# Performance work log

Hardware: AMD Instinct MI355X
Metric: run time of the kernel (lower is better)

The kernel has to match this reference:

```python
import jax, jax.numpy as jnp
import numpy as np

B, C, H, W = 32, 64, 128, 128

def setup_inputs() -> dict:
    key = jax.random.key(0)
    k1, k2, k3, k4 = jax.random.split(key, 4)
    x = jax.random.normal(k1, (B, C, H, W), dtype=jnp.float32)
    theta = jax.random.normal(k2, (C, C), dtype=jnp.float32) * (6.0 / (C + C)) ** 0.5  # xavier-ish
    W_lin = jax.random.normal(k3, (C, C), dtype=jnp.float32) * (1.0 / C) ** 0.5
    b_lin = jax.random.normal(k4, (C,), dtype=jnp.float32) * 0.01
    return {"x": x, "theta": theta, "W_lin": W_lin, "b_lin": b_lin}

def reference(x, theta, W_lin, b_lin):
    b, c, h, w = x.shape
    # channel descriptor: global average pool -> [B, C]
    wvec = jnp.mean(x, axis=(2, 3))
    # pairwise diff and soft adjacency, batched over B
    diff = wvec[:, :, None] - wvec[:, None, :]              # [B, C, C]
    e = jnp.exp(-diff)
    T = jnp.abs(1.0 - e / (1.0 + e)) - 1.0                  # [B, C, C]
    A = 0.5 * (T + jnp.swapaxes(T, 1, 2)) * theta           # [B, C, C]
    # graph conv: A @ x_flat, relu
    x_flat = x.reshape(b, c, h * w)                         # [B, C, HW]
    Hmat = jax.nn.relu(jnp.einsum('bij,bjn->bin', A, x_flat))  # [B, C, HW]
    # Linear over channel dim applied to H.T: [B, HW, C]
    Hout = jnp.einsum('bin,ci->bnc', Hmat, W_lin) + b_lin   # [B, HW, C]
    # faithful to torch: H.view(C, h, w) is a raw row-major reshape of [HW, C]
    return Hout.reshape(b, c, h, w)
```

## Files before the change

### kernel.cpp

```cpp
#include <hip/hip_runtime.h>

static constexpr int Cc  = 64;
static constexpr int HWc = 16384;
static constexpr int Bc  = 32;
static constexpr int TPX = 32;
static constexpr int TT  = 4;


typedef _Float16 v8h __attribute__((ext_vector_type(8)));
typedef float    v4f __attribute__((ext_vector_type(4)));

union FragU { uint32_t u[4]; v8h h; };

__device__ inline uint32_t packf2(float lo, float hi) {
  union { _Float16 h[2]; uint32_t u; } r;
  r.h[0] = (_Float16)lo; r.h[1] = (_Float16)hi;
  return r.u;
}

__device__ inline v4f mfma16(v8h a, v8h b, v4f c) {
  return __builtin_amdgcn_mfma_f32_16x16x32_f16(a, b, c, 0, 0, 0);
}

__device__ inline void gload_lds16(const float* g, float* l) {
  __builtin_amdgcn_global_load_lds(
      (const __attribute__((address_space(1))) void*)g,
      (__attribute__((address_space(3))) void*)l, 16, 0, 0);
}

__global__ void prep_weights(const float* __restrict__ theta,
                             const float* __restrict__ Wlin,
                             _Float16* __restrict__ M1h,
                             _Float16* __restrict__ Wh) {
  int t = blockIdx.x * 256 + threadIdx.x;
  if (t < Cc * Cc) {
    M1h[t] = (_Float16)(-0.5f * theta[t]);
    Wh[t]  = (_Float16)(Wlin[t]);
  }
}

__global__ __launch_bounds__(256, 3) void fused_mfma(
    const float* __restrict__ x,
    const _Float16* __restrict__ M1h,
    const _Float16* __restrict__ Wh,
    const float* __restrict__ blin,
    float* __restrict__ out)
{
  __shared__ __align__(16) float    xa[4][64][32];
  __shared__ __align__(16) _Float16 p2[4][32][80];

  const int tid  = threadIdx.x;
  const int wv   = tid >> 6;
  const int l    = tid & 63;
  const int lq   = tid & 15;
  const int quad = l >> 4;

  const int b     = blockIdx.x >> 5;
  const int npix0 = (blockIdx.x & 31) * 512 + wv * (TT * TPX);
  const float* xb = x + (size_t)b * Cc * HWc;

  const int gch = l >> 3;
  const int gpx = (l & 7) * 4;

  const v8h* M1v = (const v8h*)M1h;
  const v8h* Whv = (const v8h*)Wh;
  v8h w1[4][2], w2[4][2];
#pragma unroll
  for (int it = 0; it < 4; ++it)
#pragma unroll
    for (int kt = 0; kt < 2; ++kt) {
      w1[it][kt] = M1v[(it * 16 + lq) * 8 + kt * 4 + quad];
      w2[it][kt] = Whv[(it * 16 + lq) * 8 + kt * 4 + quad];
    }
  v4f bias4[4];
#pragma unroll
  for (int ct = 0; ct < 4; ++ct)
    bias4[ct] = *(const v4f*)(blin + ct * 16 + quad * 4);

#pragma unroll
  for (int i = 0; i < 8; ++i)
    gload_lds16(xb + (size_t)(i * 8 + gch) * HWc + npix0 + gpx, &xa[wv][i * 8][0]);

#pragma unroll
  for (int t = 0; t < TT; ++t) {
    const int n0 = npix0 + t * TPX;

    float f[2][2][4][2];
#pragma unroll
    for (int nt = 0; nt < 2; ++nt)
#pragma unroll
      for (int kt = 0; kt < 2; ++kt)
#pragma unroll
        for (int r = 0; r < 4; ++r) {
          const int c = kt * 16 + quad * 4 + r;
          f[nt][kt][r][0] = xa[wv][2 * c][nt * 16 + lq];
          f[nt][kt][r][1] = xa[wv][2 * c + 1][nt * 16 + lq];
        }
    asm volatile("s_waitcnt lgkmcnt(0)" ::: "memory");
    __builtin_amdgcn_sched_barrier(0);

    if (t + 1 < TT) {
#pragma unroll
      for (int i = 0; i < 8; ++i)
        gload_lds16(xb + (size_t)(i * 8 + gch) * HWc + n0 + TPX + gpx,
                    &xa[wv][i * 8][0]);
    }

#pragma unroll
    for (int nt = 0; nt < 2; ++nt) {
      FragU xf[2];
#pragma unroll
      for (int kt = 0; kt < 2; ++kt)
#pragma unroll
        for (int r = 0; r < 4; ++r)
          xf[kt].u[r] = packf2(f[nt][kt][r][0], f[nt][kt][r][1]);

#pragma unroll
      for (int it = 0; it < 4; ++it) {
        v4f a = {0.f, 0.f, 0.f, 0.f};
        a = mfma16(w1[it][0], xf[0].h, a);
        a = mfma16(w1[it][1], xf[1].h, a);
        uint2 w;
        w.x = packf2(fmaxf(a[0], 0.f), fmaxf(a[1], 0.f));
        w.y = packf2(fmaxf(a[2], 0.f), fmaxf(a[3], 0.f));
        *(uint2*)&p2[wv][nt * 16 + lq][it * 16 + quad * 4] = w;
      }

      FragU pr[2];
      pr[0].h = *(const v8h*)&p2[wv][nt * 16 + lq][quad * 8];
      pr[1].h = *(const v8h*)&p2[wv][nt * 16 + lq][32 + quad * 8];

      float* orow = out + ((size_t)b * HWc + n0 + nt * 16 + lq) * Cc + quad * 4;
#pragma unroll
      for (int ct = 0; ct < 4; ++ct) {
        v4f a = bias4[ct];
        a = mfma16(w2[ct][0], pr[0].h, a);
        a = mfma16(w2[ct][1], pr[1].h, a);
        __builtin_nontemporal_store(a, (v4f*)(orow + ct * 16));
      }
    }
  }
}

extern "C" void kernel_launch(void* const* d_in, const int* in_sizes, int n_in,
                              void* d_out, int out_size, void* d_ws, size_t ws_size,
                              hipStream_t stream) {
  const float* x     = (const float*)d_in[0];
  const float* theta = (const float*)d_in[1];
  const float* W_lin = (const float*)d_in[2];
  const float* b_lin = (const float*)d_in[3];
  float* out = (float*)d_out;

  _Float16* M1h = (_Float16*)d_ws;
  _Float16* Wh  = M1h + Cc * Cc;

  prep_weights<<<(Cc * Cc + 255) / 256, 256, 0, stream>>>(theta, W_lin, M1h, Wh);

  const int nblocks = Bc * HWc / 512;
  fused_mfma<<<nblocks, 256, 0, stream>>>(x, M1h, Wh, b_lin, out);
}
```

Before: 251.1 us.

## Restructure into block-wide double-buffered 64-pixel phases with LDS-resident weights

```diff
diff --git a/kernel.cpp b/kernel.cpp
--- a/kernel.cpp
+++ b/kernel.cpp
@@ -3,8 +3,9 @@
 static constexpr int Cc  = 64;
 static constexpr int HWc = 16384;
 static constexpr int Bc  = 32;
-static constexpr int TPX = 32;
-static constexpr int TT  = 4;
+static constexpr int PXB = 1024;
+static constexpr int PH  = 64;
+static constexpr int NPH = PXB / PH;
 
 
 typedef _Float16 v8h __attribute__((ext_vector_type(8)));
@@ -22,10 +23,10 @@
   return __builtin_amdgcn_mfma_f32_16x16x32_f16(a, b, c, 0, 0, 0);
 }
 
-__device__ inline void gload_lds16(const float* g, float* l) {
+__device__ inline void gload_lds4(const float* g, float* l) {
   __builtin_amdgcn_global_load_lds(
       (const __attribute__((address_space(1))) void*)g,
-      (__attribute__((address_space(3))) void*)l, 16, 0, 0);
+      (__attribute__((address_space(3))) void*)l, 4, 0, 0);
 }
 
 __global__ void prep_weights(const float* __restrict__ theta,
@@ -39,105 +40,109 @@
   }
 }
 
-__global__ __launch_bounds__(256, 3) void fused_mfma(
+__global__ __launch_bounds__(256) void fused_mfma(
     const float* __restrict__ x,
     const _Float16* __restrict__ M1h,
     const _Float16* __restrict__ Wh,
     const float* __restrict__ blin,
     float* __restrict__ out)
 {
-  __shared__ __align__(16) float    xa[4][64][32];
-  __shared__ __align__(16) _Float16 p2[4][32][80];
+  __shared__ __align__(16) float    xbuf[2][64][65];
+  __shared__ __align__(16) _Float16 M1l[64][72];
+  __shared__ __align__(16) _Float16 Wl [64][72];
+  __shared__ __align__(16) _Float16 p2 [4][16][72];
 
   const int tid  = threadIdx.x;
   const int wv   = tid >> 6;
   const int l    = tid & 63;
   const int lq   = tid & 15;
   const int quad = l >> 4;
+  const int pxw  = wv * 16 + lq;
 
-  const int b     = blockIdx.x >> 5;
-  const int npix0 = (blockIdx.x & 31) * 512 + wv * (TT * TPX);
+  const int b   = blockIdx.x >> 4;
+  const int px0 = (blockIdx.x & 15) * PXB;
   const float* xb = x + (size_t)b * Cc * HWc;
 
-  const int gch = l >> 3;
-  const int gpx = (l & 7) * 4;
-
-  const v8h* M1v = (const v8h*)M1h;
-  const v8h* Whv = (const v8h*)Wh;
-  v8h w1[4][2], w2[4][2];
-#pragma unroll
-  for (int it = 0; it < 4; ++it)
-#pragma unroll
-    for (int kt = 0; kt < 2; ++kt) {
-      w1[it][kt] = M1v[(it * 16 + lq) * 8 + kt * 4 + quad];
-      w2[it][kt] = Whv[(it * 16 + lq) * 8 + kt * 4 + quad];
-    }
+  {
+    const int r = tid >> 2, seg = (tid & 3) * 16;
+    const uint4 m0 = *(const uint4*)(M1h + r * 64 + seg);
+    const uint4 m1 = *(const uint4*)(M1h + r * 64 + seg + 8);
+    const uint4 w0 = *(const uint4*)(Wh  + r * 64 + seg);
+    const uint4 w1 = *(const uint4*)(Wh  + r * 64 + seg + 8);
+    *(uint4*)&M1l[r][seg]     = m0;
+    *(uint4*)&M1l[r][seg + 8] = m1;
+    *(uint4*)&Wl[r][seg]      = w0;
+    *(uint4*)&Wl[r][seg + 8]  = w1;
+  }
   v4f bias4[4];
 #pragma unroll
   for (int ct = 0; ct < 4; ++ct)
     bias4[ct] = *(const v4f*)(blin + ct * 16 + quad * 4);
 
 #pragma unroll
-  for (int i = 0; i < 8; ++i)
-    gload_lds16(xb + (size_t)(i * 8 + gch) * HWc + npix0 + gpx, &xa[wv][i * 8][0]);
+  for (int i = 0; i < 16; ++i) {
+    const int c = wv * 16 + i;
+    gload_lds4(xb + (size_t)c * HWc + px0 + l, &xbuf[0][c][0]);
+  }
+
+  __syncthreads();
+
+  for (int t = 0; t < NPH; ++t) {
+    if (t < NPH - 1) {
+      const int pb = px0 + (t + 1) * PH;
+      float* dst = &xbuf[(t + 1) & 1][0][0];
+#pragma unroll
+      for (int i = 0; i < 16; ++i) {
+        const int c = wv * 16 + i;
+        gload_lds4(xb + (size_t)c * HWc + pb + l, dst + c * 65);
+      }
+      __builtin_amdgcn_sched_barrier(0);
+    }
+
+    const int kb = t & 1;
+    FragU xf[2];
+#pragma unroll
+    for (int kt = 0; kt < 2; ++kt)
+#pragma unroll
+      for (int r = 0; r < 4; ++r) {
+        const int c0 = kt * 32 + quad * 8 + 2 * r;
+        xf[kt].u[r] = packf2(xbuf[kb][c0][pxw], xbuf[kb][c0 + 1][pxw]);
+      }
 
 #pragma unroll
-  for (int t = 0; t < TT; ++t) {
-    const int n0 = npix0 + t * TPX;
-
-    float f[2][2][4][2];
-#pragma unroll
-    for (int nt = 0; nt < 2; ++nt)
+    for (int it = 0; it < 4; ++it) {
+      v4f a = {0.f, 0.f, 0.f, 0.f};
 #pragma unroll
       for (int kt = 0; kt < 2; ++kt)
-#pragma unroll
-        for (int r = 0; r < 4; ++r) {
-          const int c = kt * 16 + quad * 4 + r;
-          f[nt][kt][r][0] = xa[wv][2 * c][nt * 16 + lq];
-          f[nt][kt][r][1] = xa[wv][2 * c + 1][nt * 16 + lq];
-        }
-    asm volatile("s_waitcnt lgkmcnt(0)" ::: "memory");
-    __builtin_amdgcn_sched_barrier(0);
-
-    if (t + 1 < TT) {
-#pragma unroll
-      for (int i = 0; i < 8; ++i)
-        gload_lds16(xb + (size_t)(i * 8 + gch) * HWc + n0 + TPX + gpx,
-                    &xa[wv][i * 8][0]);
+        a = mfma16(*(const v8h*)&M1l[it * 16 + lq][kt * 32 + quad * 8],
+                   xf[kt].h, a);
+      uint2 w;
+      w.x = packf2(fmaxf(a[0], 0.f), fmaxf(a[1], 0.f));
+      w.y = packf2(fmaxf(a[2], 0.f), fmaxf(a[3], 0.f));
+      *(uint2*)&p2[wv][lq][it * 16 + quad * 4] = w;
     }
 
+    FragU pr[2];
 #pragma unroll
-    for (int nt = 0; nt < 2; ++nt) {
-      FragU xf[2];
+    for (int kt = 0; kt < 2; ++kt)
+      pr[kt].h = *(const v8h*)&p2[wv][lq][kt * 32 + quad * 8];
+
+    float* orow = out + ((size_t)b * HWc + px0 + t * PH + pxw) * Cc + quad * 4;
+#pragma unroll
+    for (int ct = 0; ct < 4; ++ct) {
+      v4f a = bias4[ct];
 #pragma unroll
       for (int kt = 0; kt < 2; ++kt)
-#pragma unroll
-        for (int r = 0; r < 4; ++r)
-          xf[kt].u[r] = packf2(f[nt][kt][r][0], f[nt][kt][r][1]);
+        a = mfma16(*(const v8h*)&Wl[ct * 16 + lq][kt * 32 + quad * 8],
+                   pr[kt].h, a);
+      *(v4f*)(orow + ct * 16) = a;
+    }
 
-#pragma unroll
-      for (int it = 0; it < 4; ++it) {
-        v4f a = {0.f, 0.f, 0.f, 0.f};
-        a = mfma16(w1[it][0], xf[0].h, a);
-        a = mfma16(w1[it][1], xf[1].h, a);
-        uint2 w;
-        w.x = packf2(fmaxf(a[0], 0.f), fmaxf(a[1], 0.f));
-        w.y = packf2(fmaxf(a[2], 0.f), fmaxf(a[3], 0.f));
-        *(uint2*)&p2[wv][nt * 16 + lq][it * 16 + quad * 4] = w;
-      }
-
-      FragU pr[2];
-      pr[0].h = *(const v8h*)&p2[wv][nt * 16 + lq][quad * 8];
-      pr[1].h = *(const v8h*)&p2[wv][nt * 16 + lq][32 + quad * 8];
-
-      float* orow = out + ((size_t)b * HWc + n0 + nt * 16 + lq) * Cc + quad * 4;
-#pragma unroll
-      for (int ct = 0; ct < 4; ++ct) {
-        v4f a = bias4[ct];
-        a = mfma16(w2[ct][0], pr[0].h, a);
-        a = mfma16(w2[ct][1], pr[1].h, a);
-        __builtin_nontemporal_store(a, (v4f*)(orow + ct * 16));
-      }
+    if (t < NPH - 1) {
+      asm volatile("s_waitcnt vmcnt(4)" ::: "memory");
+      __builtin_amdgcn_sched_barrier(0);
+      __builtin_amdgcn_s_barrier();
+      __builtin_amdgcn_sched_barrier(0);
     }
   }
 }
@@ -156,6 +161,6 @@
 
   prep_weights<<<(Cc * Cc + 255) / 256, 256, 0, stream>>>(theta, W_lin, M1h, Wh);
 
-  const int nblocks = Bc * HWc / 512;
+  const int nblocks = Bc * HWc / PXB;
   fused_mfma<<<nblocks, 256, 0, stream>>>(x, M1h, Wh, b_lin, out);
 }
```

Measured after the change: 258.8 us. +3.1%, slower.
